# Kernel tuning notes

Hardware: AMD Instinct MI355X
Metric: run time of the kernel (lower is better)

The kernel has to match this reference:

```python
import jax, jax.numpy as jnp
import numpy as np

# torch.optim.Adam defaults
LR = 1e-3
B1 = 0.9
B2 = 0.999
EPS = 1e-8


def setup_inputs() -> dict:
    key = jax.random.key(0)
    k1, k2 = jax.random.split(key)
    B, N_train, d = 128, 16384, 1024
    h = jax.random.normal(k1, (B, d), dtype=jnp.float32)
    H_train = jax.random.normal(k2, (N_train, d), dtype=jnp.float32)
    return {"h": h, "H_train": H_train, "n_epoch": 1000}


def reference(h, H_train, n_epoch):
    # preweights: [B, N_train], optimized by Adam for n_epoch steps
    B, N_train = h.shape[0], H_train.shape[0]

    def loss_fn(p):
        w = jax.nn.softmax(p, axis=-1)          # [B, N_train]
        H_approx = w @ H_train                   # [B, d]
        return jnp.sum((H_approx - h) ** 2)

    grad_fn = jax.grad(loss_fn)

    def step(carry, t):
        p, m, v = carry
        g = grad_fn(p)
        m = B1 * m + (1.0 - B1) * g
        v = B2 * v + (1.0 - B2) * (g * g)
        m_hat = m / (1.0 - B1 ** t)
        v_hat = v / (1.0 - B2 ** t)
        p = p - LR * m_hat / (jnp.sqrt(v_hat) + EPS)
        return (p, m, v), None

    z = jnp.zeros((B, N_train), dtype=jnp.float32)
    ts = jnp.arange(1, n_epoch + 1, dtype=jnp.float32)
    (p, _, _), _ = jax.lax.scan(step, (z, z, z), ts)
    return jax.nn.softmax(p, axis=-1)
```

## Files before the change

### kernel.cpp

```cpp
#include <hip/hip_runtime.h>
#include <math.h>

#define BB 128
#define NTR 16384
#define DD 1024
#define PN (BB*NTR)
#define CN (BB*DD)
#define HN (NTR*DD)
#define FWD_SLABS 64
#define BWD_SLABS 2

typedef short bf16x8 __attribute__((ext_vector_type(8)));
typedef float f32x2  __attribute__((ext_vector_type(2)));
typedef float f32x4v __attribute__((ext_vector_type(4)));

__device__ __forceinline__ ushort f2bf(float f) {
  uint u = __float_as_uint(f);
  return (ushort)((u + 0x7FFFu + ((u >> 16) & 1u)) >> 16);
}
__device__ __forceinline__ float bf2f(ushort h) { return __uint_as_float(((uint)h) << 16); }
__device__ __forceinline__ void split2(float f, ushort& a, ushort& b) {
  a = f2bf(f); float r1 = f - bf2f(a);
  b = f2bf(r1);
}

__global__ __launch_bounds__(256) void k_prep(const float* __restrict__ H,
    ushort* __restrict__ H0, ushort* __restrict__ H1)
{
  const size_t i = ((size_t)blockIdx.x * 256 + threadIdx.x) * 4;
  const float4 x = *(const float4*)(H + i);
  ushort a[4], b[4];
  split2(x.x, a[0], b[0]); split2(x.y, a[1], b[1]);
  split2(x.z, a[2], b[2]); split2(x.w, a[3], b[3]);
  *(ushort4*)(H0 + i) = make_ushort4(a[0], a[1], a[2], a[3]);
  *(ushort4*)(H1 + i) = make_ushort4(b[0], b[1], b[2], b[3]);
}

__global__ __launch_bounds__(512) void k_softmax_f(const float* __restrict__ p,
                                                   float* __restrict__ w) {
  const int row = blockIdx.x, tid = threadIdx.x;
  const float* pr = p + (size_t)row * NTR;
  float x[32]; float mx = -INFINITY;
#pragma unroll
  for (int i = 0; i < 32; ++i) { x[i] = pr[i*512 + tid]; mx = fmaxf(mx, x[i]); }
  __shared__ float red[512];
  red[tid] = mx; __syncthreads();
  for (int s = 256; s > 0; s >>= 1) { if (tid < s) red[tid] = fmaxf(red[tid], red[tid+s]); __syncthreads(); }
  mx = red[0]; __syncthreads();
  float sum = 0.f;
#pragma unroll
  for (int i = 0; i < 32; ++i) { x[i] = expf(x[i] - mx); sum += x[i]; }
  red[tid] = sum; __syncthreads();
  for (int s = 256; s > 0; s >>= 1) { if (tid < s) red[tid] += red[tid+s]; __syncthreads(); }
  const float inv = 1.0f / red[0];
  float* wr = w + (size_t)row * NTR;
#pragma unroll
  for (int i = 0; i < 32; ++i) wr[i*512 + tid] = x[i] * inv;
}

__global__ __launch_bounds__(256) void k_fwd_v(const float* __restrict__ w,
    const float* __restrict__ H, float* __restrict__ Cp)
{
  const int nt = blockIdx.x, tid = threadIdx.x;
  const int kbase = blockIdx.y * 256;
  Cp += (size_t)blockIdx.y * CN;
  __shared__ float As[8][128];
  __shared__ float Bs[8][128];
  const int tm = tid >> 4, tn = tid & 15;
  const int m0 = tm * 8, n0 = tn * 8;
  const int mm = tid >> 1, q = tid & 1;
  const int br = tid >> 5, bc = (tid & 31) * 4;
  const float* Asrc = w + (size_t)mm*NTR + kbase + q*4;
  const float* Bsrc = H + (size_t)(kbase+br)*DD + nt*128 + bc;

  f32x2 acc[8][4];
#pragma unroll
  for (int i = 0; i < 8; ++i)
#pragma unroll
    for (int j = 0; j < 4; ++j) acc[i][j] = (f32x2){0.f, 0.f};

  float4 ra = *(const float4*)(Asrc);
  float4 rb = *(const float4*)(Bsrc);
  for (int kk = 0; kk < 256; kk += 8) {
    __syncthreads();
    As[q*4+0][mm]=ra.x; As[q*4+1][mm]=ra.y; As[q*4+2][mm]=ra.z; As[q*4+3][mm]=ra.w;
    *(float4*)&Bs[br][bc] = rb;
    __syncthreads();
    if (kk + 8 < 256) {
      ra = *(const float4*)(Asrc + kk + 8);
      rb = *(const float4*)(Bsrc + (size_t)(kk+8)*DD);
    }
#pragma unroll
    for (int k = 0; k < 8; ++k) {
      float a[8];
      *(float4*)&a[0] = *(const float4*)&As[k][m0];
      *(float4*)&a[4] = *(const float4*)&As[k][m0+4];
      f32x2 b[4];
      b[0] = *(const f32x2*)&Bs[k][n0];
      b[1] = *(const f32x2*)&Bs[k][n0+2];
      b[2] = *(const f32x2*)&Bs[k][n0+4];
      b[3] = *(const f32x2*)&Bs[k][n0+6];
#pragma unroll
      for (int i = 0; i < 8; ++i) {
        const f32x2 ai = (f32x2){a[i], a[i]};
#pragma unroll
        for (int j = 0; j < 4; ++j)
          acc[i][j] = __builtin_elementwise_fma(ai, b[j], acc[i][j]);
      }
    }
  }
#pragma unroll
  for (int i = 0; i < 8; ++i) {
    float* dst = Cp + (size_t)(m0+i)*DD + nt*128 + n0;
    *(float4*)dst     = make_float4(acc[i][0].x, acc[i][0].y, acc[i][1].x, acc[i][1].y);
    *(float4*)(dst+4) = make_float4(acc[i][2].x, acc[i][2].y, acc[i][3].x, acc[i][3].y);
  }
}

__global__ __launch_bounds__(256) void k_reduce_S2s(const float* __restrict__ X,
    const float* __restrict__ h,
    ushort* __restrict__ s0, ushort* __restrict__ s1)
{
  const size_t off = ((size_t)blockIdx.x * 256 + threadIdx.x) * 2;
  f32x2 s = (f32x2){0.f, 0.f};
#pragma unroll 4
  for (int k = 0; k < FWD_SLABS; ++k) {
    const f32x2 c = *(const f32x2*)(X + (size_t)k * CN + off);
    s.x += c.x; s.y += c.y;
  }
  const f32x2 hh = *(const f32x2*)(h + off);
  float v0 = 2.f*(s.x-hh.x), v1 = 2.f*(s.y-hh.y);
  ushort a0, b0, a1, b1;
  split2(v0, a0, b0); split2(v1, a1, b1);
  *(ushort2*)(s0 + off) = make_ushort2(a0, a1);
  *(ushort2*)(s1 + off) = make_ushort2(b0, b1);
}

__global__ __launch_bounds__(256, 2) void k_gemm3_bwd(
    const ushort* __restrict__ A0, const ushort* __restrict__ A1,
    const ushort* __restrict__ B0, const ushort* __restrict__ B1,
    const float* __restrict__ w,
    float* __restrict__ C, float* __restrict__ rpart)
{
  __shared__ ushort lds[12288];
  __shared__ float rbuf[128][33];
  const int tid = threadIdx.x;
  const int lane = tid & 63, wid = tid >> 6;
  const int wm = (wid >> 1) * 64, wn = (wid & 1) * 32;
  const int bn = blockIdx.x, ks = blockIdx.y;
  const int n0 = bn * 64;
  const int kbase = ks * 512;
  C += (size_t)ks * PN;

  const ushort* Ap[2] = {A0, A1};
  const ushort* Bp[2] = {B0, B1};

  f32x4v acc[4][2];
#pragma unroll
  for (int i = 0; i < 4; ++i)
#pragma unroll
    for (int j = 0; j < 2; ++j) acc[i][j] = (f32x4v){0.f, 0.f, 0.f, 0.f};

  for (int kt = 0; kt < 16; ++kt) {
    const int kpos = kbase + (kt << 5);
#pragma unroll
    for (int c = 0; c < 4; ++c) {
      const int L = c*256 + tid;
      const int s = L >> 9, rr = L & 511;
      const int row = rr >> 2, slot = rr & 3;
      const int sl = slot ^ ((row >> 1) & 3);
      const ushort* src = Ap[s] + (size_t)row * DD + kpos + (sl << 3);
      __builtin_amdgcn_global_load_lds((const __attribute__((address_space(1))) void*)src,
          (__attribute__((address_space(3))) void*)&lds[(size_t)(c*256 + (wid << 6)) * 8], 16, 0, 0);
    }
#pragma unroll
    for (int c = 0; c < 2; ++c) {
      const int L = c*256 + tid;
      const int s = L >> 8, rr = L & 255;
      const int row = rr >> 2, slot = rr & 3;
      const int sl = slot ^ ((row >> 1) & 3);
      const ushort* src = Bp[s] + (size_t)(n0 + row) * DD + kpos + (sl << 3);
      __builtin_amdgcn_global_load_lds((const __attribute__((address_space(1))) void*)src,
          (__attribute__((address_space(3))) void*)&lds[8192 + (size_t)(c*256 + (wid << 6)) * 8], 16, 0, 0);
    }
    __syncthreads();

    bf16x8 bf[2][2];
#pragma unroll
    for (int s = 0; s < 2; ++s)
#pragma unroll
      for (int j = 0; j < 2; ++j) {
        const int n = wn + j*16 + (lane & 15);
        const int sl = (lane >> 4) ^ ((n >> 1) & 3);
        bf[s][j] = *(const bf16x8*)&lds[8192 + s*2048 + n*32 + sl*8];
      }
#pragma unroll
    for (int sa = 0; sa < 2; ++sa) {
      bf16x8 af[4];
#pragma unroll
      for (int i = 0; i < 4; ++i) {
        const int mrow = wm + i*16 + (lane & 15);
        const int sl = (lane >> 4) ^ ((mrow >> 1) & 3);
        af[i] = *(const bf16x8*)&lds[sa*4096 + mrow*32 + sl*8];
      }
#pragma unroll
      for (int sb = 0; sb < 2 - sa; ++sb)
#pragma unroll
        for (int i = 0; i < 4; ++i)
#pragma unroll
          for (int j = 0; j < 2; ++j)
            acc[i][j] = __builtin_amdgcn_mfma_f32_16x16x32_bf16(af[i], bf[sb][j], acc[i][j], 0, 0, 0);
    }
    __syncthreads();
  }
#pragma unroll
  for (int i = 0; i < 4; ++i) {
    const int rbase = wm + i*16 + ((lane >> 4) << 2);
#pragma unroll
    for (int r = 0; r < 4; ++r) {
      const int row = rbase + r;
      float s = 0.f;
#pragma unroll
      for (int j = 0; j < 2; ++j) {
        const int cg = n0 + wn + j*16 + (lane & 15);
        C[(size_t)row * NTR + cg] = acc[i][j][r];
        s = fmaf(w[(size_t)row * NTR + cg], acc[i][j][r], s);
      }
      rbuf[row][((wn >> 5) << 4) + (lane & 15)] = s;
    }
  }
  __syncthreads();
  if (tid < 128) {
    float s = 0.f;
#pragma unroll
    for (int t = 0; t < 32; ++t) s += rbuf[tid][t];
    rpart[((size_t)ks*256 + bn)*128 + tid] = s;
  }
}

__global__ __launch_bounds__(256) void k_adam_f(float* __restrict__ p,
    float* __restrict__ m, float* __restrict__ v,
    const float* __restrict__ w, const float* __restrict__ X,
    const float* __restrict__ rpart, float bc1, float bc2)
{
  const int bid = blockIdx.x, tid = threadIdx.x;
  const int row = bid >> 3;
  __shared__ float red[256];
  red[tid] = rpart[(size_t)tid*128 + row] + rpart[(size_t)(tid+256)*128 + row];
  __syncthreads();
  for (int s = 128; s > 0; s >>= 1) { if (tid < s) red[tid] += red[tid+s]; __syncthreads(); }
  const float rr = red[0];
  const size_t base = (size_t)bid * 2048 + tid * 4;
#pragma unroll
  for (int part = 0; part < 2; ++part) {
    const size_t off = base + part * 1024;
    float4 u  = *(const float4*)(X + off);
    const float4 u1 = *(const float4*)(X + (size_t)PN + off);
    u.x += u1.x; u.y += u1.y; u.z += u1.z; u.w += u1.w;
    const float4 w4 = *(const float4*)(w + off);
    const float wv[4] = {w4.x, w4.y, w4.z, w4.w};
    const float uu[4] = {u.x, u.y, u.z, u.w};
    float4 p4 = *(float4*)(p + off);
    float4 m4 = *(float4*)(m + off);
    float4 v4 = *(float4*)(v + off);
    float* pp = (float*)&p4; float* mm = (float*)&m4; float* vv = (float*)&v4;
#pragma unroll
    for (int e = 0; e < 4; ++e) {
      const float g  = wv[e] * (uu[e] - rr);
      const float mn = 0.9f*mm[e] + 0.1f*g;
      const float vn = 0.999f*vv[e] + 0.001f*(g*g);
      const float mh = mn / bc1, vh = vn / bc2;
      pp[e] = pp[e] - 1e-3f * mh / (sqrtf(vh) + 1e-8f);
      mm[e] = mn; vv[e] = vn;
    }
    *(float4*)(p + off) = p4;
    *(float4*)(m + off) = m4;
    *(float4*)(v + off) = v4;
  }
}

extern "C" void kernel_launch(void* const* d_in, const int* in_sizes, int n_in,
                              void* d_out, int out_size, void* d_ws, size_t ws_size,
                              hipStream_t stream) {
  const float* h = (const float*)d_in[0];
  const float* H = (const float*)d_in[1];
  (void)in_sizes; (void)n_in; (void)out_size; (void)ws_size;
  const int n_epoch = 1000;

  float* p  = (float*)d_ws;
  float* m  = p + PN;
  float* v  = m + PN;
  float* w  = v + PN;
  float* X  = w + PN;
  float* rp = X + (size_t)4*PN;
  ushort* s0 = (ushort*)(rp + 512*128);
  ushort* s1 = s0 + CN;
  ushort* H0 = s1 + CN, *H1 = H0 + HN;

  hipMemsetAsync(p, 0, (size_t)3*PN*sizeof(float), stream);
  k_prep<<<HN/1024, 256, 0, stream>>>(H, H0, H1);

  for (int s = 1; s <= n_epoch; ++s) {
    k_softmax_f<<<BB, 512, 0, stream>>>(p, w);
    k_fwd_v<<<dim3(8, FWD_SLABS), 256, 0, stream>>>(w, H, X);
    k_reduce_S2s<<<CN/512, 256, 0, stream>>>(X, h, s0, s1);
    k_gemm3_bwd<<<dim3(256, BWD_SLABS), 256, 0, stream>>>(s0, s1, H0, H1, w, X, rp);
    const float bc1 = 1.0f - powf(0.9f,   (float)s);
    const float bc2 = 1.0f - powf(0.999f, (float)s);
    k_adam_f<<<1024, 256, 0, stream>>>(p, m, v, w, X, rp, bc1, bc2);
  }
  k_softmax_f<<<BB, 512, 0, stream>>>(p, (float*)d_out);
}
```

Before: 110.0 ms.

## Fuse softmax into consumers via per-chunk online stats computed in Adam

Removes the separate per-epoch softmax kernel and the materialized w buffer. Adam now emits per-row, per-chunk max and sum-exp partial statistics for the updated p, ping-ponged between two buffers. The forward GEMM, backward epilogue and next Adam step combine these statistics and recompute w = exp(p - max)/sum on the fly. This saves a full read/write pass over the B x N array and one launch per epoch, at the cost of extra exp evaluations in three kernels. The rpart layout is also transposed for contiguous reads in Adam.

Measured after the change: 112.5 ms. 2.3% more time.

```diff
diff --git a/kernel.cpp b/kernel.cpp
--- a/kernel.cpp
+++ b/kernel.cpp
@@ -36,6 +36,24 @@
   *(ushort4*)(H1 + i) = make_ushort4(b[0], b[1], b[2], b[3]);
 }
 
+__global__ __launch_bounds__(256) void k_stat0(float* __restrict__ pmx, float* __restrict__ psm) {
+  const int i = blockIdx.x * 256 + threadIdx.x;
+  pmx[i] = 0.f;
+  psm[i] = 2048.f;
+}
+
+__device__ __forceinline__ void combine_stats(const float* __restrict__ pmx,
+    const float* __restrict__ psm, int row, float& mx, float& inv)
+{
+  mx = -INFINITY;
+#pragma unroll
+  for (int c = 0; c < 8; ++c) mx = fmaxf(mx, pmx[c*128 + row]);
+  float s = 0.f;
+#pragma unroll
+  for (int c = 0; c < 8; ++c) s += psm[c*128 + row] * expf(pmx[c*128 + row] - mx);
+  inv = 1.0f / s;
+}
+
 __global__ __launch_bounds__(512) void k_softmax_f(const float* __restrict__ p,
                                                    float* __restrict__ w) {
   const int row = blockIdx.x, tid = threadIdx.x;
@@ -58,7 +76,8 @@
   for (int i = 0; i < 32; ++i) wr[i*512 + tid] = x[i] * inv;
 }
 
-__global__ __launch_bounds__(256) void k_fwd_v(const float* __restrict__ w,
+__global__ __launch_bounds__(256) void k_fwd_v(const float* __restrict__ p,
+    const float* __restrict__ pmx, const float* __restrict__ psm,
     const float* __restrict__ H, float* __restrict__ Cp)
 {
   const int nt = blockIdx.x, tid = threadIdx.x;
@@ -66,12 +85,19 @@
   Cp += (size_t)blockIdx.y * CN;
   __shared__ float As[8][128];
   __shared__ float Bs[8][128];
+  __shared__ float smx[128], sinv[128];
+  if (tid < 128) {
+    float mx, inv; combine_stats(pmx, psm, tid, mx, inv);
+    smx[tid] = mx; sinv[tid] = inv;
+  }
   const int tm = tid >> 4, tn = tid & 15;
   const int m0 = tm * 8, n0 = tn * 8;
   const int mm = tid >> 1, q = tid & 1;
   const int br = tid >> 5, bc = (tid & 31) * 4;
-  const float* Asrc = w + (size_t)mm*NTR + kbase + q*4;
+  const float* Asrc = p + (size_t)mm*NTR + kbase + q*4;
   const float* Bsrc = H + (size_t)(kbase+br)*DD + nt*128 + bc;
+  __syncthreads();
+  const float mxv = smx[mm], invv = sinv[mm];
 
   f32x2 acc[8][4];
 #pragma unroll
@@ -81,14 +107,18 @@
 
   float4 ra = *(const float4*)(Asrc);
   float4 rb = *(const float4*)(Bsrc);
+  float4 wa = make_float4(expf(ra.x-mxv)*invv, expf(ra.y-mxv)*invv,
+                          expf(ra.z-mxv)*invv, expf(ra.w-mxv)*invv);
   for (int kk = 0; kk < 256; kk += 8) {
     __syncthreads();
-    As[q*4+0][mm]=ra.x; As[q*4+1][mm]=ra.y; As[q*4+2][mm]=ra.z; As[q*4+3][mm]=ra.w;
+    As[q*4+0][mm]=wa.x; As[q*4+1][mm]=wa.y; As[q*4+2][mm]=wa.z; As[q*4+3][mm]=wa.w;
     *(float4*)&Bs[br][bc] = rb;
     __syncthreads();
     if (kk + 8 < 256) {
       ra = *(const float4*)(Asrc + kk + 8);
       rb = *(const float4*)(Bsrc + (size_t)(kk+8)*DD);
+      wa = make_float4(expf(ra.x-mxv)*invv, expf(ra.y-mxv)*invv,
+                       expf(ra.z-mxv)*invv, expf(ra.w-mxv)*invv);
     }
 #pragma unroll
     for (int k = 0; k < 8; ++k) {
@@ -139,11 +169,13 @@
 __global__ __launch_bounds__(256, 2) void k_gemm3_bwd(
     const ushort* __restrict__ A0, const ushort* __restrict__ A1,
     const ushort* __restrict__ B0, const ushort* __restrict__ B1,
-    const float* __restrict__ w,
+    const float* __restrict__ p,
+    const float* __restrict__ pmx, const float* __restrict__ psm,
     float* __restrict__ C, float* __restrict__ rpart)
 {
   __shared__ ushort lds[12288];
   __shared__ float rbuf[128][33];
+  __shared__ float smx[128], sinv[128];
   const int tid = threadIdx.x;
   const int lane = tid & 63, wid = tid >> 6;
   const int wm = (wid >> 1) * 64, wn = (wid & 1) * 32;
@@ -213,18 +245,25 @@
     }
     __syncthreads();
   }
+  if (tid < 128) {
+    float mx, inv; combine_stats(pmx, psm, tid, mx, inv);
+    smx[tid] = mx; sinv[tid] = inv;
+  }
+  __syncthreads();
 #pragma unroll
   for (int i = 0; i < 4; ++i) {
     const int rbase = wm + i*16 + ((lane >> 4) << 2);
 #pragma unroll
     for (int r = 0; r < 4; ++r) {
       const int row = rbase + r;
+      const float mxv = smx[row], invv = sinv[row];
       float s = 0.f;
 #pragma unroll
       for (int j = 0; j < 2; ++j) {
         const int cg = n0 + wn + j*16 + (lane & 15);
         C[(size_t)row * NTR + cg] = acc[i][j][r];
-        s = fmaf(w[(size_t)row * NTR + cg], acc[i][j][r], s);
+        const float wv = expf(p[(size_t)row * NTR + cg] - mxv) * invv;
+        s = fmaf(wv, acc[i][j][r], s);
       }
       rbuf[row][((wn >> 5) << 4) + (lane & 15)] = s;
     }
@@ -234,48 +273,68 @@
     float s = 0.f;
 #pragma unroll
     for (int t = 0; t < 32; ++t) s += rbuf[tid][t];
-    rpart[((size_t)ks*256 + bn)*128 + tid] = s;
-  }
-}
-
-__global__ __launch_bounds__(256) void k_adam_f(float* __restrict__ p,
+    rpart[(size_t)tid * 512 + ks*256 + bn] = s;
+  }
+}
+
+__global__ __launch_bounds__(256) void k_adam_f(float* __restrict__ pp_,
     float* __restrict__ m, float* __restrict__ v,
-    const float* __restrict__ w, const float* __restrict__ X,
-    const float* __restrict__ rpart, float bc1, float bc2)
+    const float* __restrict__ X, const float* __restrict__ rpart,
+    const float* __restrict__ pmx_in, const float* __restrict__ psm_in,
+    float* __restrict__ pmx_out, float* __restrict__ psm_out,
+    float bc1, float bc2)
 {
   const int bid = blockIdx.x, tid = threadIdx.x;
-  const int row = bid >> 3;
+  const int row = bid >> 3, chunk = bid & 7;
+  float mx, inv; combine_stats(pmx_in, psm_in, row, mx, inv);
   __shared__ float red[256];
-  red[tid] = rpart[(size_t)tid*128 + row] + rpart[(size_t)(tid+256)*128 + row];
+  red[tid] = rpart[(size_t)row*512 + tid] + rpart[(size_t)row*512 + 256 + tid];
   __syncthreads();
   for (int s = 128; s > 0; s >>= 1) { if (tid < s) red[tid] += red[tid+s]; __syncthreads(); }
   const float rr = red[0];
   const size_t base = (size_t)bid * 2048 + tid * 4;
+  float pn[8];
 #pragma unroll
   for (int part = 0; part < 2; ++part) {
     const size_t off = base + part * 1024;
     float4 u  = *(const float4*)(X + off);
     const float4 u1 = *(const float4*)(X + (size_t)PN + off);
     u.x += u1.x; u.y += u1.y; u.z += u1.z; u.w += u1.w;
-    const float4 w4 = *(const float4*)(w + off);
-    const float wv[4] = {w4.x, w4.y, w4.z, w4.w};
     const float uu[4] = {u.x, u.y, u.z, u.w};
-    float4 p4 = *(float4*)(p + off);
+    float4 p4 = *(float4*)(pp_ + off);
     float4 m4 = *(float4*)(m + off);
     float4 v4 = *(float4*)(v + off);
     float* pp = (float*)&p4; float* mm = (float*)&m4; float* vv = (float*)&v4;
 #pragma unroll
     for (int e = 0; e < 4; ++e) {
-      const float g  = wv[e] * (uu[e] - rr);
+      const float wv = expf(pp[e] - mx) * inv;
+      const float g  = wv * (uu[e] - rr);
       const float mn = 0.9f*mm[e] + 0.1f*g;
       const float vn = 0.999f*vv[e] + 0.001f*(g*g);
       const float mh = mn / bc1, vh = vn / bc2;
       pp[e] = pp[e] - 1e-3f * mh / (sqrtf(vh) + 1e-8f);
       mm[e] = mn; vv[e] = vn;
-    }
-    *(float4*)(p + off) = p4;
+      pn[part*4 + e] = pp[e];
+    }
+    *(float4*)(pp_ + off) = p4;
     *(float4*)(m + off) = m4;
     *(float4*)(v + off) = v4;
+  }
+  float lmx = pn[0];
+#pragma unroll
+  for (int e = 1; e < 8; ++e) lmx = fmaxf(lmx, pn[e]);
+  __syncthreads();
+  red[tid] = lmx; __syncthreads();
+  for (int s = 128; s > 0; s >>= 1) { if (tid < s) red[tid] = fmaxf(red[tid], red[tid+s]); __syncthreads(); }
+  const float bmx = red[0]; __syncthreads();
+  float ls = 0.f;
+#pragma unroll
+  for (int e = 0; e < 8; ++e) ls += expf(pn[e] - bmx);
+  red[tid] = ls; __syncthreads();
+  for (int s = 128; s > 0; s >>= 1) { if (tid < s) red[tid] += red[tid+s]; __syncthreads(); }
+  if (tid == 0) {
+    pmx_out[chunk*128 + row] = bmx;
+    psm_out[chunk*128 + row] = red[0];
   }
 }
 
@@ -290,24 +349,31 @@
   float* p  = (float*)d_ws;
   float* m  = p + PN;
   float* v  = m + PN;
-  float* w  = v + PN;
-  float* X  = w + PN;
+  float* X  = v + PN;
   float* rp = X + (size_t)4*PN;
-  ushort* s0 = (ushort*)(rp + 512*128);
+  float* pmxA = rp + 128*512;
+  float* psmA = pmxA + 1024;
+  float* pmxB = psmA + 1024;
+  float* psmB = pmxB + 1024;
+  ushort* s0 = (ushort*)(psmB + 1024);
   ushort* s1 = s0 + CN;
   ushort* H0 = s1 + CN, *H1 = H0 + HN;
 
   hipMemsetAsync(p, 0, (size_t)3*PN*sizeof(float), stream);
   k_prep<<<HN/1024, 256, 0, stream>>>(H, H0, H1);
+  k_stat0<<<4, 256, 0, stream>>>(pmxA, psmA);
 
   for (int s = 1; s <= n_epoch; ++s) {
-    k_softmax_f<<<BB, 512, 0, stream>>>(p, w);
-    k_fwd_v<<<dim3(8, FWD_SLABS), 256, 0, stream>>>(w, H, X);
+    float* pmx_in  = (s & 1) ? pmxA : pmxB;
+    float* psm_in  = (s & 1) ? psmA : psmB;
+    float* pmx_out = (s & 1) ? pmxB : pmxA;
+    float* psm_out = (s & 1) ? psmB : psmA;
+    k_fwd_v<<<dim3(8, FWD_SLABS), 256, 0, stream>>>(p, pmx_in, psm_in, H, X);
     k_reduce_S2s<<<CN/512, 256, 0, stream>>>(X, h, s0, s1);
-    k_gemm3_bwd<<<dim3(256, BWD_SLABS), 256, 0, stream>>>(s0, s1, H0, H1, w, X, rp);
+    k_gemm3_bwd<<<dim3(256, BWD_SLABS), 256, 0, stream>>>(s0, s1, H0, H1, p, pmx_in, psm_in, X, rp);
     const float bc1 = 1.0f - powf(0.9f,   (float)s);
     const float bc2 = 1.0f - powf(0.999f, (float)s);
-    k_adam_f<<<1024, 256, 0, stream>>>(p, m, v, w, X, rp, bc1, bc2);
+    k_adam_f<<<1024, 256, 0, stream>>>(p, m, v, X, rp, pmx_in, psm_in, pmx_out, psm_out, bc1, bc2);
   }
   k_softmax_f<<<BB, 512, 0, stream>>>(p, (float*)d_out);
 }
```
